# Performance work log

Measured on AMD Instinct MI355X. Metric: run time of the kernel, lower is better.

## Reference

```python
import jax, jax.numpy as jnp
import numpy as np

ALPHA = 0.5
BETA = 5.0
LOGIT_SCALE = 100.0  # exp(log(100)) -- CLIP's learned logit scale at its clamp value
NUM_CLASSES = 200


def _l2norm(x):
    return x / jnp.linalg.norm(x, axis=-1, keepdims=True)


def setup_inputs() -> dict:
    key = jax.random.key(0)
    k1, k2, k3, k4 = jax.random.split(key, 4)
    img_f = jax.random.normal(k1, (1024, 512), dtype=jnp.float32)
    text_features = jax.random.normal(k2, (200, 512), dtype=jnp.float32)
    keys = jax.random.normal(k3, (50000, 512), dtype=jnp.float32)
    labels = jax.random.randint(k4, (50000,), 0, NUM_CLASSES, dtype=jnp.int64)
    return {"img_f": img_f, "text_features": text_features, "keys": keys, "labels": labels}


def reference(img_f, text_features, keys, labels):
    # encode_image output is L2-normalized in the module; keys were built from
    # normalized image features, text_features are normalized class embeddings.
    q = _l2norm(img_f)            # [B, D]
    t = _l2norm(text_features)    # [C, D]
    k = _l2norm(keys)             # [N, D]

    # CLIP zero-shot branch: scale * q @ t.T -> [B, C]
    z = LOGIT_SCALE * jnp.einsum('bd,cd->bc', q, t)

    # Tip-Adapter cache branch: exp(beta * q @ keys.T) @ one_hot(labels)
    sim = jnp.einsum('bd,nd->bn', q, k)                 # [B, N]
    aff = jnp.exp(BETA * sim)                           # [B, N]
    values = jax.nn.one_hot(labels, NUM_CLASSES, dtype=aff.dtype)  # [N, C]
    c = aff @ values                                    # [B, C]

    return (1.0 - ALPHA) * z + ALPHA * c
```

## Files before the change

kernel.cpp:

```cpp
#include <hip/hip_runtime.h>

#define B_Q    1024
#define D_K    512
#define N_CLS  200
#define N_KEYS 50000
#define N_PAD  50048
#define N_EXT  (N_PAD + 256)
#define N_ZT   (N_PAD / 128)

typedef __attribute__((ext_vector_type(8))) short bf16x8;
typedef __attribute__((ext_vector_type(4))) float f32x4;

__device__ __forceinline__ unsigned short f2bf(float f) {
  union { float f; unsigned int i; } v; v.f = f;
  unsigned int r = v.i + 0x7fffu + ((v.i >> 16) & 1u);
  return (unsigned short)(r >> 16);
}
__device__ __forceinline__ uint4 pack8(const float f[8], float s) {
  uint4 o;
  o.x = (unsigned)f2bf(f[0]*s) | ((unsigned)f2bf(f[1]*s) << 16);
  o.y = (unsigned)f2bf(f[2]*s) | ((unsigned)f2bf(f[3]*s) << 16);
  o.z = (unsigned)f2bf(f[4]*s) | ((unsigned)f2bf(f[5]*s) << 16);
  o.w = (unsigned)f2bf(f[6]*s) | ((unsigned)f2bf(f[7]*s) << 16);
  return o;
}
__device__ __forceinline__ void async_copy16(const void* g, void* lds) {
  __builtin_amdgcn_global_load_lds(
      (const __attribute__((address_space(1))) unsigned int*)g,
      (__attribute__((address_space(3))) unsigned int*)lds, 16, 0, 0);
}

__global__ void k_hist(const int* __restrict__ labels, int* __restrict__ hist) {
  __shared__ int h[N_CLS];
  int t = threadIdx.x;
  if (t < N_CLS) h[t] = 0;
  __syncthreads();
  int n = blockIdx.x * 256 + t;
  if (n < N_KEYS) atomicAdd(&h[labels[n]], 1);
  __syncthreads();
  if (t < N_CLS && h[t]) atomicAdd(&hist[t], h[t]);
}

__global__ void k_scan(const int* __restrict__ hist, int* __restrict__ cursor) {
  __shared__ int s[N_CLS];
  int t = threadIdx.x;
  int v = (t < N_CLS) ? hist[t] : 0;
  if (t < N_CLS) s[t] = v;
  __syncthreads();
  for (int d = 1; d < N_CLS; d <<= 1) {
    int x = 0;
    if (t < N_CLS && t >= d) x = s[t - d];
    __syncthreads();
    if (t < N_CLS) s[t] += x;
    __syncthreads();
  }
  if (t < N_CLS) cursor[t] = s[t] - v;
}

__global__ void k_perm(const int* __restrict__ labels, int* __restrict__ cursor,
                       int* __restrict__ dest) {
  __shared__ int lh[N_CLS];
  __shared__ int lbase[N_CLS];
  int t = threadIdx.x;
  if (t < N_CLS) lh[t] = 0;
  __syncthreads();
  int n = blockIdx.x * 256 + t;
  bool valid = (n < N_KEYS);
  int l = 0, lo = 0;
  if (valid) { l = labels[n]; lo = atomicAdd(&lh[l], 1); }
  __syncthreads();
  if (t < N_CLS && lh[t] > 0) lbase[t] = atomicAdd(&cursor[t], lh[t]);
  __syncthreads();
  if (valid) dest[n] = lbase[l] + lo;
}

__global__ void k_prep2(const float* __restrict__ keys, const float* __restrict__ img,
                        const float* __restrict__ txt, const int* __restrict__ labels,
                        const int* __restrict__ dest, unsigned short* __restrict__ qn,
                        unsigned short* __restrict__ kn, int* __restrict__ cls) {
  int w = threadIdx.x >> 6, lane = threadIdx.x & 63;
  int row = blockIdx.x * 4 + w;
  const float* src; unsigned short* dst; int r;
  if (row < N_PAD) {
    if (row >= N_KEYS) {
      *((uint4*)(kn + (size_t)row * D_K) + lane) = make_uint4(0, 0, 0, 0);
      if (lane == 0) cls[row] = N_CLS;
      return;
    }
    int d = dest[row];
    if (lane == 0) cls[d] = labels[row];
    src = keys + (size_t)row * D_K;
    dst = kn + (size_t)d * D_K;
  } else if (row < N_PAD + B_Q) {
    r = row - N_PAD;
    src = img + (size_t)r * D_K;
    dst = qn + (size_t)r * D_K;
  } else if (row < N_PAD + B_Q + N_CLS) {
    r = row - N_PAD - B_Q;
    src = txt + (size_t)r * D_K;
    dst = kn + (size_t)(N_PAD + r) * D_K;
  } else if (row < N_PAD + B_Q + N_CLS + 56) {
    r = N_PAD + N_CLS + (row - N_PAD - B_Q - N_CLS);
    *((uint4*)(kn + (size_t)r * D_K) + lane) = make_uint4(0, 0, 0, 0);
    return;
  } else return;
  const float4* s4 = (const float4*)src + lane * 2;
  float4 a = s4[0], b = s4[1];
  float f[8] = {a.x, a.y, a.z, a.w, b.x, b.y, b.z, b.w};
  float ss = 0.f;
#pragma unroll
  for (int i = 0; i < 8; i++) ss += f[i] * f[i];
#pragma unroll
  for (int d = 1; d < 64; d <<= 1) ss += __shfl_xor(ss, d);
  float rinv = rsqrtf(ss);
  *((uint4*)dst + lane) = pack8(f, rinv);
}

__global__ __launch_bounds__(256, 2) void k_main(const unsigned short* __restrict__ qn,
                                                 const unsigned short* __restrict__ kn,
                                                 const int* __restrict__ cls,
                                                 float* __restrict__ out) {
  __shared__ unsigned short As[2][128 * 64];
  __shared__ unsigned short Bs[2][128 * 64];
  int t = threadIdx.x;
  int tileB = blockIdx.x, tileN = blockIdx.y;
  int rowB0 = tileB * 128, rowN0 = tileN * 128;

  f32x4 acc[4][4];
#pragma unroll
  for (int i = 0; i < 4; i++)
#pragma unroll
    for (int j = 0; j < 4; j++) acc[i][j] = (f32x4){0.f, 0.f, 0.f, 0.f};

  int lane = t & 63, w = t >> 6;
  int wr = (w >> 1) * 64, wc = (w & 1) * 64;
  int l15 = lane & 15, lq = lane >> 4;
  const int rA = t >> 3;
  const int gsw = ((t & 7) ^ (rA & 7)) * 8;
  const int sw = l15 & 7;

#pragma unroll
  for (int i = 0; i < 4; i++) {
    int row = i * 32 + rA;
    async_copy16(qn + (size_t)(rowB0 + row) * D_K + gsw, &As[0][i * 2048 + t * 8]);
    async_copy16(kn + (size_t)(rowN0 + row) * D_K + gsw, &Bs[0][i * 2048 + t * 8]);
  }

  for (int kt = 0; kt < 8; kt++) {
    int cur = kt & 1;
    __syncthreads();
    if (kt < 7) {
      int nxt = cur ^ 1, k0 = (kt + 1) * 64;
#pragma unroll
      for (int i = 0; i < 4; i++) {
        int row = i * 32 + rA;
        async_copy16(qn + (size_t)(rowB0 + row) * D_K + k0 + gsw, &As[nxt][i * 2048 + t * 8]);
        async_copy16(kn + (size_t)(rowN0 + row) * D_K + k0 + gsw, &Bs[nxt][i * 2048 + t * 8]);
      }
    }
#pragma unroll
    for (int ks = 0; ks < 64; ks += 32) {
      bf16x8 af[4], bf[4];
#pragma unroll
      for (int i = 0; i < 4; i++)
        af[i] = *(const bf16x8*)&As[cur][(wr + 16 * i + l15) * 64 + ((((ks >> 3) + lq) ^ sw) * 8)];
#pragma unroll
      for (int j = 0; j < 4; j++)
        bf[j] = *(const bf16x8*)&Bs[cur][(wc + 16 * j + l15) * 64 + ((((ks >> 3) + lq) ^ sw) * 8)];
#pragma unroll
      for (int i = 0; i < 4; i++)
#pragma unroll
        for (int j = 0; j < 4; j++)
          acc[i][j] = __builtin_amdgcn_mfma_f32_16x16x32_bf16(af[i], bf[j], acc[i][j], 0, 0, 0);
    }
  }

  if (tileN >= N_ZT) {
#pragma unroll
    for (int i = 0; i < 4; i++)
#pragma unroll
      for (int j = 0; j < 4; j++) {
        int col = rowN0 + wc + 16 * j + l15 - N_PAD;
        if (col < N_CLS) {
#pragma unroll
          for (int r = 0; r < 4; r++) {
            int row = rowB0 + wr + 16 * i + lq * 4 + r;
            atomicAdd(out + (size_t)row * N_CLS + col, 50.0f * acc[i][j][r]);
          }
        }
      }
    return;
  }

#pragma unroll
  for (int i = 0; i < 4; i++)
#pragma unroll
    for (int j = 0; j < 4; j++)
#pragma unroll
      for (int r = 0; r < 4; r++) acc[i][j][r] = __expf(5.0f * acc[i][j][r]);

  int cj[4];
#pragma unroll
  for (int j = 0; j < 4; j++) cj[j] = cls[rowN0 + wc + 16 * j + l15];
  int cseg0 = cls[rowN0 + wc];
  int cseg1 = cls[rowN0 + wc + 63];

  for (int c = cseg0; c <= cseg1; c++) {
    if (c >= N_CLS) break;
#pragma unroll
    for (int i = 0; i < 4; i++) {
      float s0 = 0.f, s1 = 0.f, s2 = 0.f, s3 = 0.f;
#pragma unroll
      for (int j = 0; j < 4; j++) {
        if (cj[j] == c) {
          s0 += acc[i][j][0]; s1 += acc[i][j][1];
          s2 += acc[i][j][2]; s3 += acc[i][j][3];
        }
      }
#pragma unroll
      for (int d = 1; d < 16; d <<= 1) {
        s0 += __shfl_xor(s0, d); s1 += __shfl_xor(s1, d);
        s2 += __shfl_xor(s2, d); s3 += __shfl_xor(s3, d);
      }
      if (l15 == 0) {
        int row = rowB0 + wr + 16 * i + lq * 4;
        float* o = out + (size_t)row * N_CLS + c;
        if (s0 != 0.f) atomicAdd(o + 0 * N_CLS, 0.5f * s0);
        if (s1 != 0.f) atomicAdd(o + 1 * N_CLS, 0.5f * s1);
        if (s2 != 0.f) atomicAdd(o + 2 * N_CLS, 0.5f * s2);
        if (s3 != 0.f) atomicAdd(o + 3 * N_CLS, 0.5f * s3);
      }
    }
  }
}

extern "C" void kernel_launch(void* const* d_in, const int* in_sizes, int n_in,
                              void* d_out, int out_size, void* d_ws, size_t ws_size,
                              hipStream_t stream) {
  (void)in_sizes; (void)n_in; (void)out_size; (void)ws_size;
  const float* img    = (const float*)d_in[0];
  const float* txt    = (const float*)d_in[1];
  const float* keys   = (const float*)d_in[2];
  const int*   labels = (const int*)d_in[3];
  float*       out    = (float*)d_out;

  char* ws = (char*)d_ws;
  unsigned short* qn = (unsigned short*)(ws + 0);
  unsigned short* kn = (unsigned short*)(ws + 1048576);
  int*  dest   = (int*)(ws + 52559872);
  int*  cls    = (int*)(ws + 52760064);
  int*  hist   = (int*)(ws + 52960256);
  int*  cursor = (int*)(ws + 52961280);

  hipMemsetAsync(hist, 0, 256 * sizeof(int), stream);
  hipMemsetAsync(out, 0, (size_t)B_Q * N_CLS * sizeof(float), stream);

  k_hist<<<196, 256, 0, stream>>>(labels, hist);
  k_scan<<<1, 256, 0, stream>>>(hist, cursor);
  k_perm<<<196, 256, 0, stream>>>(labels, cursor, dest);
  k_prep2<<<(N_PAD + B_Q + N_CLS + 56 + 3) / 4, 256, 0, stream>>>(
      keys, img, txt, labels, dest, qn, kn, cls);
  k_main<<<dim3(B_Q / 128, N_ZT + 2), 256, 0, stream>>>(qn, kn, cls, out);
}
```

Baseline: 297.4 us.

## Merge sort kernels, fold output zeroing into prep, single-buffer main GEMM

Replaces the histogram, scan and permutation kernels and two memsets with one single-block counting-sort kernel. Output zeroing moves into the prep kernel, so fewer launches are needed. The main GEMM kernel drops LDS double buffering for a single buffer with load-then-sync, which targets 3 blocks per CU instead of 2, and it hoists the class-label loads ahead of the loop. The trade-off is lost load/compute overlap inside each block and a serial single-block sort over 50k labels.

Measured after the change: 295.4 us. About the same (-0.6%).

```diff
diff --git a/kernel.cpp b/kernel.cpp
--- a/kernel.cpp
+++ b/kernel.cpp
@@ -5,8 +5,13 @@
 #define N_CLS  200
 #define N_KEYS 50000
 #define N_PAD  50048
-#define N_EXT  (N_PAD + 256)
 #define N_ZT   (N_PAD / 128)
+
+#define R0 N_PAD
+#define R1 (R0 + B_Q)
+#define R2 (R1 + N_CLS)
+#define R3 (R2 + 56)
+#define R4 (R3 + 400)
 
 typedef __attribute__((ext_vector_type(8))) short bf16x8;
 typedef __attribute__((ext_vector_type(4))) float f32x4;
@@ -30,58 +35,40 @@
       (__attribute__((address_space(3))) unsigned int*)lds, 16, 0, 0);
 }
 
-__global__ void k_hist(const int* __restrict__ labels, int* __restrict__ hist) {
-  __shared__ int h[N_CLS];
+__global__ __launch_bounds__(1024) void k_sort(const int* __restrict__ labels,
+                                               int* __restrict__ dest) {
+  __shared__ int hist[N_CLS];
+  __shared__ int incl[N_CLS];
+  __shared__ int cur[N_CLS];
   int t = threadIdx.x;
-  if (t < N_CLS) h[t] = 0;
-  __syncthreads();
-  int n = blockIdx.x * 256 + t;
-  if (n < N_KEYS) atomicAdd(&h[labels[n]], 1);
-  __syncthreads();
-  if (t < N_CLS && h[t]) atomicAdd(&hist[t], h[t]);
-}
-
-__global__ void k_scan(const int* __restrict__ hist, int* __restrict__ cursor) {
-  __shared__ int s[N_CLS];
-  int t = threadIdx.x;
-  int v = (t < N_CLS) ? hist[t] : 0;
-  if (t < N_CLS) s[t] = v;
+  if (t < N_CLS) hist[t] = 0;
+  __syncthreads();
+  for (int n = t; n < N_KEYS; n += 1024) atomicAdd(&hist[labels[n]], 1);
+  __syncthreads();
+  if (t < N_CLS) incl[t] = hist[t];
   __syncthreads();
   for (int d = 1; d < N_CLS; d <<= 1) {
     int x = 0;
-    if (t < N_CLS && t >= d) x = s[t - d];
-    __syncthreads();
-    if (t < N_CLS) s[t] += x;
-    __syncthreads();
-  }
-  if (t < N_CLS) cursor[t] = s[t] - v;
-}
-
-__global__ void k_perm(const int* __restrict__ labels, int* __restrict__ cursor,
-                       int* __restrict__ dest) {
-  __shared__ int lh[N_CLS];
-  __shared__ int lbase[N_CLS];
-  int t = threadIdx.x;
-  if (t < N_CLS) lh[t] = 0;
-  __syncthreads();
-  int n = blockIdx.x * 256 + t;
-  bool valid = (n < N_KEYS);
-  int l = 0, lo = 0;
-  if (valid) { l = labels[n]; lo = atomicAdd(&lh[l], 1); }
-  __syncthreads();
-  if (t < N_CLS && lh[t] > 0) lbase[t] = atomicAdd(&cursor[t], lh[t]);
-  __syncthreads();
-  if (valid) dest[n] = lbase[l] + lo;
+    if (t < N_CLS && t >= d) x = incl[t - d];
+    __syncthreads();
+    if (t < N_CLS) incl[t] += x;
+    __syncthreads();
+  }
+  if (t < N_CLS) cur[t] = incl[t] - hist[t];
+  __syncthreads();
+  for (int n = t; n < N_KEYS; n += 1024)
+    dest[n] = atomicAdd(&cur[labels[n]], 1);
 }
 
 __global__ void k_prep2(const float* __restrict__ keys, const float* __restrict__ img,
                         const float* __restrict__ txt, const int* __restrict__ labels,
                         const int* __restrict__ dest, unsigned short* __restrict__ qn,
-                        unsigned short* __restrict__ kn, int* __restrict__ cls) {
+                        unsigned short* __restrict__ kn, int* __restrict__ cls,
+                        float* __restrict__ out) {
   int w = threadIdx.x >> 6, lane = threadIdx.x & 63;
   int row = blockIdx.x * 4 + w;
-  const float* src; unsigned short* dst; int r;
-  if (row < N_PAD) {
+  const float* src; unsigned short* dst;
+  if (row < R0) {
     if (row >= N_KEYS) {
       *((uint4*)(kn + (size_t)row * D_K) + lane) = make_uint4(0, 0, 0, 0);
       if (lane == 0) cls[row] = N_CLS;
@@ -91,17 +78,25 @@
     if (lane == 0) cls[d] = labels[row];
     src = keys + (size_t)row * D_K;
     dst = kn + (size_t)d * D_K;
-  } else if (row < N_PAD + B_Q) {
-    r = row - N_PAD;
+  } else if (row < R1) {
+    int r = row - R0;
     src = img + (size_t)r * D_K;
     dst = qn + (size_t)r * D_K;
-  } else if (row < N_PAD + B_Q + N_CLS) {
-    r = row - N_PAD - B_Q;
+  } else if (row < R2) {
+    int r = row - R1;
+    if (lane == 0) cls[N_PAD + r] = N_CLS;
     src = txt + (size_t)r * D_K;
     dst = kn + (size_t)(N_PAD + r) * D_K;
-  } else if (row < N_PAD + B_Q + N_CLS + 56) {
-    r = N_PAD + N_CLS + (row - N_PAD - B_Q - N_CLS);
+  } else if (row < R3) {
+    int r = N_PAD + N_CLS + (row - R2);
     *((uint4*)(kn + (size_t)r * D_K) + lane) = make_uint4(0, 0, 0, 0);
+    if (lane == 0) cls[r] = N_CLS;
+    return;
+  } else if (row < R4) {
+    int zr = row - R3;
+    uint4* o4 = (uint4*)(out + (size_t)zr * 512) + lane * 2;
+    o4[0] = make_uint4(0, 0, 0, 0);
+    o4[1] = make_uint4(0, 0, 0, 0);
     return;
   } else return;
   const float4* s4 = (const float4*)src + lane * 2;
@@ -116,12 +111,12 @@
   *((uint4*)dst + lane) = pack8(f, rinv);
 }
 
-__global__ __launch_bounds__(256, 2) void k_main(const unsigned short* __restrict__ qn,
+__global__ __launch_bounds__(256, 3) void k_main(const unsigned short* __restrict__ qn,
                                                  const unsigned short* __restrict__ kn,
                                                  const int* __restrict__ cls,
                                                  float* __restrict__ out) {
-  __shared__ unsigned short As[2][128 * 64];
-  __shared__ unsigned short Bs[2][128 * 64];
+  __shared__ unsigned short As[128 * 64];
+  __shared__ unsigned short Bs[128 * 64];
   int t = threadIdx.x;
   int tileB = blockIdx.x, tileN = blockIdx.y;
   int rowB0 = tileB * 128, rowN0 = tileN * 128;
@@ -139,34 +134,30 @@
   const int gsw = ((t & 7) ^ (rA & 7)) * 8;
   const int sw = l15 & 7;
 
-#pragma unroll
-  for (int i = 0; i < 4; i++) {
-    int row = i * 32 + rA;
-    async_copy16(qn + (size_t)(rowB0 + row) * D_K + gsw, &As[0][i * 2048 + t * 8]);
-    async_copy16(kn + (size_t)(rowN0 + row) * D_K + gsw, &Bs[0][i * 2048 + t * 8]);
-  }
-
-  for (int kt = 0; kt < 8; kt++) {
-    int cur = kt & 1;
-    __syncthreads();
-    if (kt < 7) {
-      int nxt = cur ^ 1, k0 = (kt + 1) * 64;
-#pragma unroll
-      for (int i = 0; i < 4; i++) {
-        int row = i * 32 + rA;
-        async_copy16(qn + (size_t)(rowB0 + row) * D_K + k0 + gsw, &As[nxt][i * 2048 + t * 8]);
-        async_copy16(kn + (size_t)(rowN0 + row) * D_K + k0 + gsw, &Bs[nxt][i * 2048 + t * 8]);
-      }
-    }
+  int cj[4];
+#pragma unroll
+  for (int j = 0; j < 4; j++) cj[j] = cls[rowN0 + wc + 16 * j + l15];
+  int cseg0 = cls[rowN0 + wc];
+  int cseg1 = cls[rowN0 + wc + 63];
+
+  for (int k0 = 0; k0 < D_K; k0 += 64) {
+    __syncthreads();
+#pragma unroll
+    for (int i = 0; i < 4; i++) {
+      int row = i * 32 + rA;
+      async_copy16(qn + (size_t)(rowB0 + row) * D_K + k0 + gsw, &As[i * 2048 + t * 8]);
+      async_copy16(kn + (size_t)(rowN0 + row) * D_K + k0 + gsw, &Bs[i * 2048 + t * 8]);
+    }
+    __syncthreads();
 #pragma unroll
     for (int ks = 0; ks < 64; ks += 32) {
       bf16x8 af[4], bf[4];
 #pragma unroll
       for (int i = 0; i < 4; i++)
-        af[i] = *(const bf16x8*)&As[cur][(wr + 16 * i + l15) * 64 + ((((ks >> 3) + lq) ^ sw) * 8)];
+        af[i] = *(const bf16x8*)&As[(wr + 16 * i + l15) * 64 + ((((ks >> 3) + lq) ^ sw) * 8)];
 #pragma unroll
       for (int j = 0; j < 4; j++)
-        bf[j] = *(const bf16x8*)&Bs[cur][(wc + 16 * j + l15) * 64 + ((((ks >> 3) + lq) ^ sw) * 8)];
+        bf[j] = *(const bf16x8*)&Bs[(wc + 16 * j + l15) * 64 + ((((ks >> 3) + lq) ^ sw) * 8)];
 #pragma unroll
       for (int i = 0; i < 4; i++)
 #pragma unroll
@@ -198,12 +189,6 @@
     for (int j = 0; j < 4; j++)
 #pragma unroll
       for (int r = 0; r < 4; r++) acc[i][j][r] = __expf(5.0f * acc[i][j][r]);
-
-  int cj[4];
-#pragma unroll
-  for (int j = 0; j < 4; j++) cj[j] = cls[rowN0 + wc + 16 * j + l15];
-  int cseg0 = cls[rowN0 + wc];
-  int cseg1 = cls[rowN0 + wc + 63];
 
   for (int c = cseg0; c <= cseg1; c++) {
     if (c >= N_CLS) break;
@@ -247,18 +232,10 @@
   char* ws = (char*)d_ws;
   unsigned short* qn = (unsigned short*)(ws + 0);
   unsigned short* kn = (unsigned short*)(ws + 1048576);
-  int*  dest   = (int*)(ws + 52559872);
-  int*  cls    = (int*)(ws + 52760064);
-  int*  hist   = (int*)(ws + 52960256);
-  int*  cursor = (int*)(ws + 52961280);
-
-  hipMemsetAsync(hist, 0, 256 * sizeof(int), stream);
-  hipMemsetAsync(out, 0, (size_t)B_Q * N_CLS * sizeof(float), stream);
-
-  k_hist<<<196, 256, 0, stream>>>(labels, hist);
-  k_scan<<<1, 256, 0, stream>>>(hist, cursor);
-  k_perm<<<196, 256, 0, stream>>>(labels, cursor, dest);
-  k_prep2<<<(N_PAD + B_Q + N_CLS + 56 + 3) / 4, 256, 0, stream>>>(
-      keys, img, txt, labels, dest, qn, kn, cls);
+  int*  dest = (int*)(ws + 52559872);
+  int*  cls  = (int*)(ws + 52760064);
+
+  k_sort<<<1, 1024, 0, stream>>>(labels, dest);
+  k_prep2<<<(R4 + 3) / 4, 256, 0, stream>>>(keys, img, txt, labels, dest, qn, kn, cls, out);
   k_main<<<dim3(B_Q / 128, N_ZT + 2), 256, 0, stream>>>(qn, kn, cls, out);
 }
```
